# Kernel optimization log

Measured on AMD Instinct MI355X. Metric: run time of the kernel, lower is better.

Reference implementation:

```python
import jax, jax.numpy as jnp
import numpy as np

B, T, C, H = 4, 2048, 768, 768  # batch, seq, embed_size, embed_size_h


def setup_inputs() -> dict:
    key = jax.random.key(0)
    ks = jax.random.split(key, 7)
    s = 1.0 / np.sqrt(C)  # torch Linear default-ish init scale
    return {
        "x": jax.random.normal(ks[0], (B, T, C), jnp.float32),
        "Wq": jax.random.normal(ks[1], (C, H), jnp.float32) * s,
        "bq": jnp.zeros((H,), jnp.float32),
        "Wk": jax.random.normal(ks[2], (C, H), jnp.float32) * s,
        "bk": jnp.zeros((H,), jnp.float32),
        "Wv": jax.random.normal(ks[3], (C, H), jnp.float32) * s,
        "bv": jnp.zeros((H,), jnp.float32),
    }


def reference(x, Wq, bq, Wk, bk, Wv, bv):
    # q,k,v: [B,T,H]
    q = x @ Wq + bq
    k = x @ Wk + bk
    v = x @ Wv + bv
    scale = jnp.asarray(H, x.dtype) ** -0.5
    # full [B,T,T] score matrix, as the original module does
    qk = jnp.einsum("btd,bsd->bts", q, k) * scale
    tril = jnp.tril(jnp.ones((T, T), x.dtype))
    qk = qk * tril
    # original quirk: masked_fill on exact zeros (covers upper triangle)
    qk = jnp.where(qk == 0, -jnp.inf, qk)
    attn = jax.nn.softmax(qk, axis=-1)  # [B,T,T]
    # note: in the source, dropout is applied to a dead value; output uses softmax directly
    return attn @ v  # [B,T,H]
```

## Files before the change

### kernel.cpp

```cpp
#include <hip/hip_runtime.h>
#include <math.h>


#define BB 4
#define TT 2048
#define CC 768

typedef __bf16 bf16_t;
typedef __bf16 bf16x8 __attribute__((ext_vector_type(8)));
typedef _Float16 half8 __attribute__((ext_vector_type(8)));
typedef float f32x4 __attribute__((ext_vector_type(4)));

__device__ __forceinline__ void async_load16(void* lds, const void* g) {
  __builtin_amdgcn_global_load_lds(
      (const __attribute__((address_space(1))) void*)g,
      (__attribute__((address_space(3))) void*)lds, 16, 0, 0);
}

__device__ __forceinline__ void stage_tile64(const bf16_t* __restrict__ g0,
                                             int ld, bf16_t* lds, int t) {
  int w = t >> 6, l = t & 63;
#pragma unroll
  for (int i = 0; i < 4; ++i) {
    int c = i * 256 + w * 64 + l;
    int row = c >> 3;
    int p = c & 7;
    int q = p ^ (row & 7);
    async_load16(lds + i * 2048 + w * 512,
                 g0 + row * ld + q * 8);
  }
}

__device__ __forceinline__ bf16x8 read_frag64(const bf16_t* lds, int r, int q) {
  int p = q ^ (r & 7);
  return *(const bf16x8*)(lds + r * 64 + p * 8);
}

__device__ __forceinline__ void mfma_tile64(const bf16_t* Ab, const bf16_t* Bb,
                                            int wr, int wc, int l,
                                            f32x4 acc[4][4]) {
  int qq = l >> 4;
#pragma unroll
  for (int half = 0; half < 2; ++half) {
    int q = half * 4 + qq;
    bf16x8 af[4], bfr[4];
#pragma unroll
    for (int i = 0; i < 4; ++i) {
      af[i] = read_frag64(Ab, wr + i * 16 + (l & 15), q);
      bfr[i] = read_frag64(Bb, wc + i * 16 + (l & 15), q);
    }
#pragma unroll
    for (int mi = 0; mi < 4; ++mi)
#pragma unroll
      for (int ni = 0; ni < 4; ++ni)
        acc[mi][ni] = __builtin_amdgcn_mfma_f32_16x16x32_bf16(
            af[mi], bfr[ni], acc[mi][ni], 0, 0, 0);
  }
}

__device__ __forceinline__ void gemm_core(const bf16_t* __restrict__ A, int lda,
                                          const bf16_t* __restrict__ B, int ldb,
                                          int kTiles64, bf16_t* As, bf16_t* Bs,
                                          f32x4 acc[4][4]) {
  int t = threadIdx.x;
  int l = t & 63;
  int w = t >> 6;
  int wr = (w >> 1) * 64;
  int wc = (w & 1) * 64;

  for (int kt = 0; kt < kTiles64; ++kt) {
    __syncthreads();
    stage_tile64(A + kt * 64, lda, As, t);
    stage_tile64(B + kt * 64, ldb, Bs, t);
    __syncthreads();
    mfma_tile64(As, Bs, wr, wc, l, acc);
  }
}


__global__ __launch_bounds__(256) void cast_x_kernel(
    const float* __restrict__ x, bf16_t* __restrict__ xbf) {
  int i = blockIdx.x * 256 + threadIdx.x;
  const float4* xin = (const float4*)x;
  float4 a = xin[i * 2];
  float4 b = xin[i * 2 + 1];
  bf16_t tmp[8];
  tmp[0] = (bf16_t)a.x; tmp[1] = (bf16_t)a.y;
  tmp[2] = (bf16_t)a.z; tmp[3] = (bf16_t)a.w;
  tmp[4] = (bf16_t)b.x; tmp[5] = (bf16_t)b.y;
  tmp[6] = (bf16_t)b.z; tmp[7] = (bf16_t)b.w;
  *(uint4*)(xbf + (size_t)i * 8) = *(const uint4*)tmp;
}

__global__ __launch_bounds__(256) void transpose_w_kernel(
    const float* __restrict__ Wq, const float* __restrict__ Wk,
    const float* __restrict__ Wv, bf16_t* __restrict__ wt) {
  int z = blockIdx.z;
  const float* W = (z == 0) ? Wq : (z == 1) ? Wk : Wv;
  bf16_t* out = wt + (size_t)z * CC * CC;
  __shared__ float tile[32][33];
  int tx = threadIdx.x;
  int ty = threadIdx.y;
  int n0 = blockIdx.x * 32;
  int c0 = blockIdx.y * 32;
#pragma unroll
  for (int k = 0; k < 4; ++k)
    tile[ty + k * 8][tx] = W[(size_t)(c0 + ty + k * 8) * CC + n0 + tx];
  __syncthreads();
#pragma unroll
  for (int k = 0; k < 4; ++k)
    out[(size_t)(n0 + ty + k * 8) * CC + c0 + tx] =
        (bf16_t)tile[tx][ty + k * 8];
}

__global__ __launch_bounds__(256) void qkv_gemm_kernel(
    const bf16_t* __restrict__ xbf, const bf16_t* __restrict__ wt,
    const float* __restrict__ bq, const float* __restrict__ bk,
    const float* __restrict__ bv, bf16_t* __restrict__ qb,
    bf16_t* __restrict__ kb, bf16_t* __restrict__ vt) {
  __shared__ bf16_t As[128 * 64];
  __shared__ bf16_t Bs[128 * 64];
  int n0 = blockIdx.x * 128;
  int m0 = blockIdx.y * 128;
  int z = blockIdx.z;

  f32x4 acc[4][4];
#pragma unroll
  for (int i = 0; i < 4; ++i)
#pragma unroll
    for (int j = 0; j < 4; ++j) acc[i][j] = (f32x4){0.f, 0.f, 0.f, 0.f};

  const bf16_t* A = xbf + (size_t)m0 * CC;
  const bf16_t* B = wt + (size_t)z * CC * CC + (size_t)n0 * CC;
  gemm_core(A, CC, B, CC, CC / 64, As, Bs, acc);

  int l = threadIdx.x & 63, w = threadIdx.x >> 6;
  int wr = (w >> 1) * 64, wc = (w & 1) * 64;
  const float* bias = (z == 0) ? bq : (z == 1) ? bk : bv;
  float scale = (z == 0) ? rsqrtf((float)CC) : 1.0f;

#pragma unroll
  for (int mi = 0; mi < 4; ++mi) {
#pragma unroll
    for (int ni = 0; ni < 4; ++ni) {
      int col = n0 + wc + ni * 16 + (l & 15);
      int rbase = m0 + wr + mi * 16 + (l >> 4) * 4;
      float bcol = bias[col];
#pragma unroll
      for (int r = 0; r < 4; ++r) {
        int m = rbase + r;
        float v = (acc[mi][ni][r] + bcol) * scale;
        bf16_t h = (bf16_t)v;
        if (z == 0) {
          qb[(size_t)m * CC + col] = h;
        } else if (z == 1) {
          kb[(size_t)m * CC + col] = h;
        } else {
          int b = m >> 11, tt = m & (TT - 1);
          vt[((size_t)b * CC + col) * TT + tt] = h;
        }
      }
    }
  }
}

__global__ __launch_bounds__(256) void s_gemm_kernel(
    const bf16_t* __restrict__ qb, const bf16_t* __restrict__ kb,
    _Float16* __restrict__ S) {
  int tj = blockIdx.x, ti = blockIdx.y, b = blockIdx.z;
  if (tj > ti) return;
  __shared__ bf16_t As[128 * 64];
  __shared__ bf16_t Bs[128 * 64];
  int m0 = ti * 128, n0 = tj * 128;

  f32x4 acc[4][4];
#pragma unroll
  for (int i = 0; i < 4; ++i)
#pragma unroll
    for (int j = 0; j < 4; ++j) acc[i][j] = (f32x4){0.f, 0.f, 0.f, 0.f};

  const bf16_t* A = qb + ((size_t)b * TT + m0) * CC;
  const bf16_t* B = kb + ((size_t)b * TT + n0) * CC;
  gemm_core(A, CC, B, CC, CC / 64, As, Bs, acc);

  _Float16* Sb = S + (size_t)b * TT * TT;
  int l = threadIdx.x & 63, w = threadIdx.x >> 6;
  int wr = (w >> 1) * 64, wc = (w & 1) * 64;
#pragma unroll
  for (int mi = 0; mi < 4; ++mi) {
#pragma unroll
    for (int ni = 0; ni < 4; ++ni) {
      int j = n0 + wc + ni * 16 + (l & 15);
      int ibase = m0 + wr + mi * 16 + (l >> 4) * 4;
#pragma unroll
      for (int r = 0; r < 4; ++r) {
        int i = ibase + r;
        float v = acc[mi][ni][r];
        if (j > i || v == 0.0f) v = -INFINITY;
        Sb[(size_t)i * TT + j] = (_Float16)v;
      }
    }
  }
}

__global__ __launch_bounds__(256) void rowstat_kernel(
    const _Float16* __restrict__ S, bf16_t* __restrict__ P) {
  int row = blockIdx.x & (TT - 1);
  int b = blockIdx.x >> 11;
  const _Float16* s = S + ((size_t)b * TT + row) * TT;
  bf16_t* p = P + ((size_t)b * TT + row) * TT;
  int pe = ((row >> 7) + 1) << 7;
  int j = threadIdx.x * 8;
  bool live = j < pe;

  float f[8];
  if (live) {
    half8 h = *(const half8*)(s + j);
#pragma unroll
    for (int k = 0; k < 8; ++k) f[k] = (float)h[k];
  } else {
#pragma unroll
    for (int k = 0; k < 8; ++k) f[k] = -INFINITY;
  }

  float m = f[0];
#pragma unroll
  for (int k = 1; k < 8; ++k) m = fmaxf(m, f[k]);
#pragma unroll
  for (int off = 32; off > 0; off >>= 1) m = fmaxf(m, __shfl_xor(m, off));
  __shared__ float redm[4];
  int w = threadIdx.x >> 6, l = threadIdx.x & 63;
  if (l == 0) redm[w] = m;
  __syncthreads();
  m = fmaxf(fmaxf(redm[0], redm[1]), fmaxf(redm[2], redm[3]));

  float e[8];
  float sum = 0.f;
#pragma unroll
  for (int k = 0; k < 8; ++k) {
    e[k] = __expf(f[k] - m);
    sum += e[k];
  }
#pragma unroll
  for (int off = 32; off > 0; off >>= 1) sum += __shfl_xor(sum, off);
  __shared__ float reds[4];
  if (l == 0) reds[w] = sum;
  __syncthreads();
  float inv = 1.0f / (reds[0] + reds[1] + reds[2] + reds[3]);

  if (live) {
    bf16x8 o;
#pragma unroll
    for (int k = 0; k < 8; ++k) o[k] = (bf16_t)(e[k] * inv);
    *(bf16x8*)(p + j) = o;
  }
}

__global__ __launch_bounds__(256) void o_gemm_kernel(
    const bf16_t* __restrict__ P, const bf16_t* __restrict__ vt,
    float* __restrict__ out) {
  int nj = blockIdx.x;
  int ti = (int)gridDim.y - 1 - (int)blockIdx.y;
  int b = blockIdx.z;
  __shared__ bf16_t As[128 * 64];
  __shared__ bf16_t Bs[128 * 64];
  int m0 = ti * 128, n0 = nj * 128;

  f32x4 acc[4][4];
#pragma unroll
  for (int i = 0; i < 4; ++i)
#pragma unroll
    for (int j = 0; j < 4; ++j) acc[i][j] = (f32x4){0.f, 0.f, 0.f, 0.f};

  const bf16_t* A = P + ((size_t)b * TT + m0) * TT;
  const bf16_t* B = vt + ((size_t)b * CC + n0) * TT;
  gemm_core(A, TT, B, TT, (ti + 1) * 2, As, Bs, acc);

  float* Ob = out + (size_t)b * TT * CC;
  int l = threadIdx.x & 63, w = threadIdx.x >> 6;
  int wr = (w >> 1) * 64, wc = (w & 1) * 64;
#pragma unroll
  for (int mi = 0; mi < 4; ++mi) {
#pragma unroll
    for (int ni = 0; ni < 4; ++ni) {
      int col = n0 + wc + ni * 16 + (l & 15);
      int ibase = m0 + wr + mi * 16 + (l >> 4) * 4;
#pragma unroll
      for (int r = 0; r < 4; ++r)
        Ob[(size_t)(ibase + r) * CC + col] = acc[mi][ni][r];
    }
  }
}

extern "C" void kernel_launch(void* const* d_in, const int* in_sizes, int n_in,
                              void* d_out, int out_size, void* d_ws,
                              size_t ws_size, hipStream_t stream) {
  const float* x = (const float*)d_in[0];
  const float* Wq = (const float*)d_in[1];
  const float* bq = (const float*)d_in[2];
  const float* Wk = (const float*)d_in[3];
  const float* bk = (const float*)d_in[4];
  const float* Wv = (const float*)d_in[5];
  const float* bv = (const float*)d_in[6];
  float* out = (float*)d_out;

  char* ws = (char*)d_ws;
  size_t off = 0;
  auto carve = [&](size_t bytes) -> char* {
    char* p = ws + off;
    off += (bytes + 255) & ~(size_t)255;
    return p;
  };
  const size_t M = (size_t)BB * TT;
  bf16_t* xbf = (bf16_t*)carve(M * CC * 2);
  bf16_t* wt  = (bf16_t*)carve(3ull * CC * CC * 2);
  bf16_t* qb  = (bf16_t*)carve(M * CC * 2);
  bf16_t* kb  = (bf16_t*)carve(M * CC * 2);
  bf16_t* vt  = (bf16_t*)carve(M * CC * 2);
  _Float16* S = (_Float16*)carve((size_t)BB * TT * TT * 2);
  bf16_t* P   = (bf16_t*)carve((size_t)BB * TT * TT * 2);
  (void)off; (void)ws_size;

  cast_x_kernel<<<(M * CC / 8 + 255) / 256, 256, 0, stream>>>(x, xbf);
  transpose_w_kernel<<<dim3(CC / 32, CC / 32, 3), dim3(32, 8, 1), 0, stream>>>(
      Wq, Wk, Wv, wt);
  qkv_gemm_kernel<<<dim3(CC / 128, M / 128, 3), 256, 0, stream>>>(
      xbf, wt, bq, bk, bv, qb, kb, vt);
  s_gemm_kernel<<<dim3(TT / 128, TT / 128, BB), 256, 0, stream>>>(qb, kb, S);
  rowstat_kernel<<<BB * TT, 256, 0, stream>>>(S, P);
  o_gemm_kernel<<<dim3(CC / 128, TT / 128, BB), 256, 0, stream>>>(P, vt, out);
}
```

Measured before the change: 246.3 us.

## Split-K balance o_gemm with atomics, compact triangular s_gemm grid, fuse prep kernels

Merges the x cast and weight transpose into one prep kernel, which also zeroes the output so it can be accumulated into. The S GEMM grid is compacted to only lower-triangular tiles, found by inverting the triangular index, so no blocks launch and exit immediately. The O GEMM splits long causal rows into up to four K-chunks of 8 tiles and combines them with float atomicAdd. The aim is to even out the triangular load imbalance, at the cost of atomic traffic, a required zero-fill, and nondeterministic summation order.

```diff
diff --git a/kernel.cpp b/kernel.cpp
--- a/kernel.cpp
+++ b/kernel.cpp
@@ -78,39 +78,49 @@
 }
 
 
-__global__ __launch_bounds__(256) void cast_x_kernel(
-    const float* __restrict__ x, bf16_t* __restrict__ xbf) {
-  int i = blockIdx.x * 256 + threadIdx.x;
-  const float4* xin = (const float4*)x;
-  float4 a = xin[i * 2];
-  float4 b = xin[i * 2 + 1];
-  bf16_t tmp[8];
-  tmp[0] = (bf16_t)a.x; tmp[1] = (bf16_t)a.y;
-  tmp[2] = (bf16_t)a.z; tmp[3] = (bf16_t)a.w;
-  tmp[4] = (bf16_t)b.x; tmp[5] = (bf16_t)b.y;
-  tmp[6] = (bf16_t)b.z; tmp[7] = (bf16_t)b.w;
-  *(uint4*)(xbf + (size_t)i * 8) = *(const uint4*)tmp;
-}
-
-__global__ __launch_bounds__(256) void transpose_w_kernel(
+__global__ __launch_bounds__(256) void prep_kernel(
+    const float* __restrict__ x, bf16_t* __restrict__ xbf,
     const float* __restrict__ Wq, const float* __restrict__ Wk,
-    const float* __restrict__ Wv, bf16_t* __restrict__ wt) {
-  int z = blockIdx.z;
-  const float* W = (z == 0) ? Wq : (z == 1) ? Wk : Wv;
-  bf16_t* out = wt + (size_t)z * CC * CC;
-  __shared__ float tile[32][33];
-  int tx = threadIdx.x;
-  int ty = threadIdx.y;
-  int n0 = blockIdx.x * 32;
-  int c0 = blockIdx.y * 32;
-#pragma unroll
-  for (int k = 0; k < 4; ++k)
-    tile[ty + k * 8][tx] = W[(size_t)(c0 + ty + k * 8) * CC + n0 + tx];
-  __syncthreads();
-#pragma unroll
-  for (int k = 0; k < 4; ++k)
-    out[(size_t)(n0 + ty + k * 8) * CC + c0 + tx] =
-        (bf16_t)tile[tx][ty + k * 8];
+    const float* __restrict__ Wv, bf16_t* __restrict__ wt,
+    float* __restrict__ out) {
+  int bid = blockIdx.x;
+  int t = threadIdx.x;
+  if (bid < 3072) {
+    int i = bid * 256 + t;
+    const float4* xin = (const float4*)x;
+    float4 a = xin[i * 2];
+    float4 b = xin[i * 2 + 1];
+    bf16_t tmp[8];
+    tmp[0] = (bf16_t)a.x; tmp[1] = (bf16_t)a.y;
+    tmp[2] = (bf16_t)a.z; tmp[3] = (bf16_t)a.w;
+    tmp[4] = (bf16_t)b.x; tmp[5] = (bf16_t)b.y;
+    tmp[6] = (bf16_t)b.z; tmp[7] = (bf16_t)b.w;
+    *(uint4*)(xbf + (size_t)i * 8) = *(const uint4*)tmp;
+  } else if (bid < 4800) {
+    int r = bid - 3072;
+    int z = r / 576;
+    int rem = r - z * 576;
+    int bx = rem % 24, by = rem / 24;
+    const float* W = (z == 0) ? Wq : (z == 1) ? Wk : Wv;
+    bf16_t* o = wt + (size_t)z * CC * CC;
+    __shared__ float tile[32][33];
+    int tx = t & 31, ty = t >> 5;
+    int n0 = bx * 32, c0 = by * 32;
+#pragma unroll
+    for (int k = 0; k < 4; ++k)
+      tile[ty + k * 8][tx] = W[(size_t)(c0 + ty + k * 8) * CC + n0 + tx];
+    __syncthreads();
+#pragma unroll
+    for (int k = 0; k < 4; ++k)
+      o[(size_t)(n0 + ty + k * 8) * CC + c0 + tx] =
+          (bf16_t)tile[tx][ty + k * 8];
+  } else {
+    int r = bid - 4800;
+    float4* o4 = (float4*)out;
+    float4 z4 = {0.f, 0.f, 0.f, 0.f};
+#pragma unroll
+    for (int k = 0; k < 4; ++k) o4[r * 1024 + k * 256 + t] = z4;
+  }
 }
 
 __global__ __launch_bounds__(256) void qkv_gemm_kernel(
@@ -167,8 +177,12 @@
 __global__ __launch_bounds__(256) void s_gemm_kernel(
     const bf16_t* __restrict__ qb, const bf16_t* __restrict__ kb,
     _Float16* __restrict__ S) {
-  int tj = blockIdx.x, ti = blockIdx.y, b = blockIdx.z;
-  if (tj > ti) return;
+  int u = blockIdx.x;
+  int ti = (int)((sqrtf(8.0f * u + 1.0f) - 1.0f) * 0.5f);
+  while ((ti + 1) * (ti + 2) / 2 <= u) ++ti;
+  while (ti * (ti + 1) / 2 > u) --ti;
+  int tj = u - ti * (ti + 1) / 2;
+  int b = blockIdx.z;
   __shared__ bf16_t As[128 * 64];
   __shared__ bf16_t Bs[128 * 64];
   int m0 = ti * 128, n0 = tj * 128;
@@ -259,9 +273,17 @@
 __global__ __launch_bounds__(256) void o_gemm_kernel(
     const bf16_t* __restrict__ P, const bf16_t* __restrict__ vt,
     float* __restrict__ out) {
-  int nj = blockIdx.x;
-  int ti = (int)gridDim.y - 1 - (int)blockIdx.y;
+  int u = 39 - (int)blockIdx.x;
+  int nj = blockIdx.y;
   int b = blockIdx.z;
+  int ti, s, ns;
+  if (u < 4)       { ti = u;                  s = 0;           ns = 1; }
+  else if (u < 12) { ti = 4 + ((u - 4) >> 1); s = (u - 4) & 1; ns = 2; }
+  else if (u < 24) { ti = 8 + (u - 12) / 3;   s = (u - 12) % 3; ns = 3; }
+  else             { ti = 12 + ((u - 24) >> 2); s = (u - 24) & 3; ns = 4; }
+  int kt0 = s * 8;
+  int ktn = min(8, (ti + 1) * 2 - kt0);
+
   __shared__ bf16_t As[128 * 64];
   __shared__ bf16_t Bs[128 * 64];
   int m0 = ti * 128, n0 = nj * 128;
@@ -272,9 +294,9 @@
 #pragma unroll
     for (int j = 0; j < 4; ++j) acc[i][j] = (f32x4){0.f, 0.f, 0.f, 0.f};
 
-  const bf16_t* A = P + ((size_t)b * TT + m0) * TT;
-  const bf16_t* B = vt + ((size_t)b * CC + n0) * TT;
-  gemm_core(A, TT, B, TT, (ti + 1) * 2, As, Bs, acc);
+  const bf16_t* A = P + ((size_t)b * TT + m0) * TT + kt0 * 64;
+  const bf16_t* B = vt + ((size_t)b * CC + n0) * TT + kt0 * 64;
+  gemm_core(A, TT, B, TT, ktn, As, Bs, acc);
 
   float* Ob = out + (size_t)b * TT * CC;
   int l = threadIdx.x & 63, w = threadIdx.x >> 6;
@@ -286,8 +308,11 @@
       int col = n0 + wc + ni * 16 + (l & 15);
       int ibase = m0 + wr + mi * 16 + (l >> 4) * 4;
 #pragma unroll
-      for (int r = 0; r < 4; ++r)
-        Ob[(size_t)(ibase + r) * CC + col] = acc[mi][ni][r];
+      for (int r = 0; r < 4; ++r) {
+        float* dst = Ob + (size_t)(ibase + r) * CC + col;
+        if (ns == 1) *dst = acc[mi][ni][r];
+        else atomicAdd(dst, acc[mi][ni][r]);
+      }
     }
   }
 }
@@ -321,12 +346,10 @@
   bf16_t* P   = (bf16_t*)carve((size_t)BB * TT * TT * 2);
   (void)off; (void)ws_size;
 
-  cast_x_kernel<<<(M * CC / 8 + 255) / 256, 256, 0, stream>>>(x, xbf);
-  transpose_w_kernel<<<dim3(CC / 32, CC / 32, 3), dim3(32, 8, 1), 0, stream>>>(
-      Wq, Wk, Wv, wt);
+  prep_kernel<<<6336, 256, 0, stream>>>(x, xbf, Wq, Wk, Wv, wt, out);
   qkv_gemm_kernel<<<dim3(CC / 128, M / 128, 3), 256, 0, stream>>>(
       xbf, wt, bq, bk, bv, qb, kb, vt);
-  s_gemm_kernel<<<dim3(TT / 128, TT / 128, BB), 256, 0, stream>>>(qb, kb, S);
+  s_gemm_kernel<<<dim3(136, 1, BB), 256, 0, stream>>>(qb, kb, S);
   rowstat_kernel<<<BB * TT, 256, 0, stream>>>(S, P);
-  o_gemm_kernel<<<dim3(CC / 128, TT / 128, BB), 256, 0, stream>>>(P, vt, out);
-}
+  o_gemm_kernel<<<dim3(40, CC / 128, BB), 256, 0, stream>>>(P, vt, out);
+}
```

Result: slower. 259.6 us (+5.4%).
